# Optimization experiments

Hardware: AMD Instinct MI355X
Metric: run time of the kernel (lower is better)

## Reference

```python
import jax, jax.numpy as jnp
import numpy as np


def setup_inputs() -> dict:
    key = jax.random.key(0)
    ks = jax.random.split(key, 8)
    B = 32768
    return {
        "x": jax.random.normal(ks[0], (B, 784), dtype=jnp.float32),
        "conv_w": jax.random.normal(ks[1], (3, 3), dtype=jnp.float32),
        "fc1_w": jax.random.normal(ks[2], (512, 676), dtype=jnp.float32) * 0.04,
        "fc1_b": jax.random.normal(ks[3], (512,), dtype=jnp.float32),
        "fc2_w": jax.random.normal(ks[4], (512, 512), dtype=jnp.float32) * 0.04,
        "fc2_b": jax.random.normal(ks[5], (512,), dtype=jnp.float32),
        "out_w": jax.random.normal(ks[6], (10, 512), dtype=jnp.float32) * 0.04,
        "out_b": jax.random.normal(ks[7], (10,), dtype=jnp.float32),
    }


def reference(x, conv_w, fc1_w, fc1_b, fc2_w, fc2_b, out_w, out_b):
    B = x.shape[0]
    img = x.reshape(B, 1, 28, 28)  # NCHW, single channel
    # Valid 3x3 cross-correlation (same math as the nested tensordot loop).
    kern = conv_w.reshape(1, 1, 3, 3)  # OIHW
    conv = jax.lax.conv_general_dilated(
        img, kern, window_strides=(1, 1), padding="VALID",
        dimension_numbers=("NCHW", "OIHW", "NCHW"))  # [B,1,26,26]
    h = conv.reshape(B, 26 * 26)
    h = jax.nn.relu(h @ fc1_w.T + fc1_b)
    h = jax.nn.relu(h @ fc2_w.T + fc2_b)
    return h @ out_w.T + out_b  # [B,10] logits
```

## Files before the change

### kernel.cpp

```cpp
#include <hip/hip_runtime.h>

typedef unsigned short ushort_t;
typedef __attribute__((ext_vector_type(8))) short bf16x8;
typedef __attribute__((ext_vector_type(4))) float f32x4;
typedef __attribute__((ext_vector_type(16))) float f32x16;

__device__ __forceinline__ unsigned short f2bf(float f) {
    union { float f; unsigned u; } v; v.f = f;
    unsigned r = v.u + 0x7FFFu + ((v.u >> 16) & 1u);
    return (unsigned short)(r >> 16);
}

__device__ __forceinline__ unsigned cvt_pk_bf16(float a, float b) {
    unsigned r;
    asm("v_cvt_pk_bf16_f32 %0, %1, %2" : "=v"(r) : "v"(a), "v"(b));
    return r;
}

__global__ __launch_bounds__(256) void prep_w(const float* __restrict__ fc1_w,
                                              const float* __restrict__ cw,
                                              const float* __restrict__ fc2_w,
                                              const float* __restrict__ out_w,
                                              ushort_t* __restrict__ W1,
                                              ushort_t* __restrict__ W2,
                                              ushort_t* __restrict__ W3) {
    const int idx = blockIdx.x * 256 + threadIdx.x;
    if (idx < 425984) {
        const int ngrp = idx / 26624;
        const int kfrag = (idx % 26624) >> 9;
        const int li = idx & 511;
        const int lane = li >> 3, e = li & 7;
        const int n = ngrp * 32 + (lane & 31);
        const int p = kfrag * 16 + (lane >> 5) * 8 + e;
        float acc = 0.f;
        if (p < 784) {
            const int pr = p / 28, pc = p % 28;
            const float* frow = &fc1_w[n * 676];
#pragma unroll
            for (int dr = 0; dr < 3; ++dr) {
                const int r = pr - dr;
                const bool rok = (unsigned)r < 26u;
                const int rc = rok ? r : 0;
#pragma unroll
                for (int dc = 0; dc < 3; ++dc) {
                    const int c = pc - dc;
                    const bool cok = (unsigned)c < 26u;
                    const int cc = cok ? c : 0;
                    const float w = (rok && cok) ? cw[dr * 3 + dc] : 0.f;
                    acc += w * frow[rc * 26 + cc];
                }
            }
        }
        W1[idx] = f2bf(acc);
    }
    if (idx < 262144) {
        const int ngrp = idx / 16384;
        const int kfrag = (idx % 16384) >> 9;
        const int li = idx & 511;
        const int lane = li >> 3, e = li & 7;
        const int n = ngrp * 32 + (lane & 31);
        const int p = kfrag * 16 + (lane >> 5) * 8 + e;
        W2[idx] = f2bf(fc2_w[n * 512 + p]);
    }
    if (idx < 16 * 512)  W3[idx] = (idx < 10 * 512) ? f2bf(out_w[idx]) : (ushort_t)0;
}

__global__ __launch_bounds__(1024, 8) void mega10(const float* __restrict__ x,
                                                  const ushort_t* __restrict__ W1,
                                                  const ushort_t* __restrict__ W2,
                                                  const ushort_t* __restrict__ W3,
                                                  const float* __restrict__ b1,
                                                  const float* __restrict__ b2,
                                                  const float* __restrict__ ob,
                                                  float* __restrict__ out) {
    extern __shared__ ushort_t smem[];
    ushort_t* xs0 = smem;
    ushort_t* hs  = smem + 4096;

    const int tid = threadIdx.x;
    const int wave = tid >> 6, lane = tid & 63;
    const int r32 = lane & 31, khalf = lane >> 5;
    const int xrow = tid >> 4, xseg = tid & 15;
    const int m0 = blockIdx.x * 64;
    const size_t ng = wave;

    const float* xgp = &x[(size_t)(m0 + xrow) * 784 + xseg * 4];
    const int xldso = xrow * 64 + (((xseg >> 1) ^ (xrow & 7)) * 8) + (xseg & 1) * 4;

    f32x16 acc[2];
#pragma unroll
    for (int a = 0; a < 2; ++a)
#pragma unroll
        for (int e = 0; e < 16; ++e) acc[a][e] = 0.f;

    f32x4 xv;
    unsigned xlo, xhi;
    auto load_x = [&](int ks) {
        const int gc = ks * 64 + xseg * 4;
        if (gc < 784) {
            xv = __builtin_nontemporal_load((const f32x4*)(xgp + ks * 64));
        } else {
            xv = (f32x4){0.f, 0.f, 0.f, 0.f};
        }
    };
    auto cvt_x = [&]() {
        xlo = cvt_pk_bf16(xv.x, xv.y);
        xhi = cvt_pk_bf16(xv.z, xv.w);
    };
    auto write_x = [&](ushort_t* buf) {
        unsigned long long v = ((unsigned long long)xhi << 32) | xlo;
        *(unsigned long long*)&buf[xldso] = v;
    };

    auto write_h = [&](const float* __restrict__ bias) {
        const int n = wave * 32 + r32;
        const float bb = bias[n];
        const int nseg = n >> 3, nrem = n & 7;
#pragma unroll
        for (int i = 0; i < 2; ++i)
#pragma unroll
            for (int reg = 0; reg < 16; ++reg) {
                const int m = i * 32 + 4 * khalf + (reg & 3) + 8 * (reg >> 2);
                hs[m * 512 + ((nseg ^ (m & 7)) * 8) + nrem] = f2bf(fmaxf(acc[i][reg] + bb, 0.f));
            }
    };

    auto p1_ksub = [&](int kf, int ksub, const ushort_t* bufp) {
        const bf16x8 bw = *(const bf16x8*)&W1[(ng * 52 + kf) * 512 + lane * 8];
        const int q = 2 * ksub + khalf;
        bf16x8 af[2];
#pragma unroll
        for (int i = 0; i < 2; ++i) {
            const int m = i * 32 + r32;
            af[i] = *(const bf16x8*)&bufp[m * 64 + ((q ^ (m & 7)) * 8)];
        }
        __builtin_amdgcn_s_setprio(1);
        acc[0] = __builtin_amdgcn_mfma_f32_32x32x16_bf16(af[0], bw, acc[0], 0, 0, 0);
        acc[1] = __builtin_amdgcn_mfma_f32_32x32x16_bf16(af[1], bw, acc[1], 0, 0, 0);
        __builtin_amdgcn_s_setprio(0);
    };

    load_x(0);
    cvt_x();
    write_x(xs0);
    __syncthreads();

    for (int ks = 0; ks < 12; ++ks) {
        load_x(ks + 1);
        const ushort_t* bufp = (ks & 1) ? hs : xs0;
        p1_ksub(ks * 4 + 0, 0, bufp);
        p1_ksub(ks * 4 + 1, 1, bufp);
        p1_ksub(ks * 4 + 2, 2, bufp);
        cvt_x();
        p1_ksub(ks * 4 + 3, 3, bufp);
        write_x((ks & 1) ? xs0 : hs);
        __syncthreads();
    }
    {
        const ushort_t* bufp = xs0;
        const bf16x8 bw = *(const bf16x8*)&W1[(ng * 52 + 48) * 512 + lane * 8];
        const int q = khalf;
        bf16x8 af[2];
#pragma unroll
        for (int i = 0; i < 2; ++i) {
            const int m = i * 32 + r32;
            af[i] = *(const bf16x8*)&bufp[m * 64 + ((q ^ (m & 7)) * 8)];
        }
        __builtin_amdgcn_s_setprio(1);
        acc[0] = __builtin_amdgcn_mfma_f32_32x32x16_bf16(af[0], bw, acc[0], 0, 0, 0);
        acc[1] = __builtin_amdgcn_mfma_f32_32x32x16_bf16(af[1], bw, acc[1], 0, 0, 0);
        __builtin_amdgcn_s_setprio(0);
    }

    write_h(b1);
#pragma unroll
    for (int a = 0; a < 2; ++a)
#pragma unroll
        for (int e = 0; e < 16; ++e) acc[a][e] = 0.f;
    __syncthreads();

    for (int ks = 0; ks < 8; ++ks) {
#pragma unroll
        for (int ksub = 0; ksub < 4; ++ksub) {
            const int kf = ks * 4 + ksub;
            const bf16x8 bw = *(const bf16x8*)&W2[(ng * 32 + kf) * 512 + lane * 8];
            const int hq = kf * 2 + khalf;
            bf16x8 af[2];
#pragma unroll
            for (int i = 0; i < 2; ++i) {
                const int m = i * 32 + r32;
                af[i] = *(const bf16x8*)&hs[m * 512 + ((hq ^ (m & 7)) * 8)];
            }
            __builtin_amdgcn_s_setprio(1);
            acc[0] = __builtin_amdgcn_mfma_f32_32x32x16_bf16(af[0], bw, acc[0], 0, 0, 0);
            acc[1] = __builtin_amdgcn_mfma_f32_32x32x16_bf16(af[1], bw, acc[1], 0, 0, 0);
            __builtin_amdgcn_s_setprio(0);
        }
    }
    __syncthreads();

    write_h(b2);
    __syncthreads();

    if (wave < 4) {
        const int quad = lane >> 4, l16 = lane & 15;
        const int row = wave * 16 + l16;
        f32x4 hacc = {0.f, 0.f, 0.f, 0.f};
#pragma unroll
        for (int ks = 0; ks < 16; ++ks) {
            const int seg = 4 * ks + quad;
            const bf16x8 a = *(const bf16x8*)&hs[row * 512 + ((seg ^ (row & 7)) * 8)];
            const bf16x8 b = *(const bf16x8*)&W3[l16 * 512 + ks * 32 + quad * 8];
            hacc = __builtin_amdgcn_mfma_f32_16x16x32_bf16(a, b, hacc, 0, 0, 0);
        }
        if (l16 < 10) {
            const float bb = ob[l16];
#pragma unroll
            for (int r = 0; r < 4; ++r)
                out[(size_t)(m0 + wave * 16 + quad * 4 + r) * 10 + l16] = hacc[r] + bb;
        }
    }
}

extern "C" void kernel_launch(void* const* d_in, const int* in_sizes, int n_in,
                              void* d_out, int out_size, void* d_ws, size_t ws_size,
                              hipStream_t stream) {
    const float* x      = (const float*)d_in[0];
    const float* conv_w = (const float*)d_in[1];
    const float* fc1_w  = (const float*)d_in[2];
    const float* fc1_b  = (const float*)d_in[3];
    const float* fc2_w  = (const float*)d_in[4];
    const float* fc2_b  = (const float*)d_in[5];
    const float* out_w  = (const float*)d_in[6];
    const float* out_b  = (const float*)d_in[7];
    float* out = (float*)d_out;

    ushort_t* W1 = (ushort_t*)d_ws;
    ushort_t* W2 = W1 + 425984;
    ushort_t* W3 = W2 + 262144;

    prep_w<<<dim3(1664), 256, 0, stream>>>(fc1_w, conv_w, fc2_w, out_w, W1, W2, W3);

    mega10<<<dim3(512), 1024, 73728, stream>>>(x, W1, W2, W3, fc1_b, fc2_b, out_b, out);
}
```

Measured before the change: 213.0 us.

## Halve rows per block to 32 to double blocks and cut LDS

Each block now handles 32 batch rows instead of 64. That halves shared memory to 36 KB and doubles the grid to 1024 blocks, so more blocks can be resident per CU. Each wave now issues one MFMA per k-fragment instead of two, so every weight fragment loaded from global memory is reused across half as many rows, roughly doubling weight traffic. The loop body is also restructured to load four weight and four activation fragments up front before the MFMA chain.

```diff
diff --git a/kernel.cpp b/kernel.cpp
--- a/kernel.cpp
+++ b/kernel.cpp
@@ -2,6 +2,7 @@
 
 typedef unsigned short ushort_t;
 typedef __attribute__((ext_vector_type(8))) short bf16x8;
+typedef __attribute__((ext_vector_type(2))) float f32x2;
 typedef __attribute__((ext_vector_type(4))) float f32x4;
 typedef __attribute__((ext_vector_type(16))) float f32x16;
 
@@ -65,7 +66,7 @@
     if (idx < 16 * 512)  W3[idx] = (idx < 10 * 512) ? f2bf(out_w[idx]) : (ushort_t)0;
 }
 
-__global__ __launch_bounds__(1024, 8) void mega10(const float* __restrict__ x,
+__global__ __launch_bounds__(1024, 8) void mega11(const float* __restrict__ x,
                                                   const ushort_t* __restrict__ W1,
                                                   const ushort_t* __restrict__ W2,
                                                   const ushort_t* __restrict__ W3,
@@ -75,41 +76,33 @@
                                                   float* __restrict__ out) {
     extern __shared__ ushort_t smem[];
     ushort_t* xs0 = smem;
-    ushort_t* hs  = smem + 4096;
+    ushort_t* hs  = smem + 2048;
 
     const int tid = threadIdx.x;
     const int wave = tid >> 6, lane = tid & 63;
     const int r32 = lane & 31, khalf = lane >> 5;
-    const int xrow = tid >> 4, xseg = tid & 15;
-    const int m0 = blockIdx.x * 64;
+    const int xrow = tid >> 5, xc2 = (tid & 31) * 2;
+    const int m0 = blockIdx.x * 32;
     const size_t ng = wave;
 
-    const float* xgp = &x[(size_t)(m0 + xrow) * 784 + xseg * 4];
-    const int xldso = xrow * 64 + (((xseg >> 1) ^ (xrow & 7)) * 8) + (xseg & 1) * 4;
-
-    f32x16 acc[2];
-#pragma unroll
-    for (int a = 0; a < 2; ++a)
-#pragma unroll
-        for (int e = 0; e < 16; ++e) acc[a][e] = 0.f;
-
-    f32x4 xv;
-    unsigned xlo, xhi;
+    const float* xgp = &x[(size_t)(m0 + xrow) * 784 + xc2];
+    const int xldso = xrow * 64 + (((xc2 >> 3) ^ (xrow & 7)) * 8) + (xc2 & 7);
+
+    f32x16 acc;
+#pragma unroll
+    for (int e = 0; e < 16; ++e) acc[e] = 0.f;
+
+    f32x2 xv;
     auto load_x = [&](int ks) {
-        const int gc = ks * 64 + xseg * 4;
+        const int gc = ks * 64 + xc2;
         if (gc < 784) {
-            xv = __builtin_nontemporal_load((const f32x4*)(xgp + ks * 64));
+            xv = __builtin_nontemporal_load((const f32x2*)(xgp + ks * 64));
         } else {
-            xv = (f32x4){0.f, 0.f, 0.f, 0.f};
-        }
-    };
-    auto cvt_x = [&]() {
-        xlo = cvt_pk_bf16(xv.x, xv.y);
-        xhi = cvt_pk_bf16(xv.z, xv.w);
+            xv = (f32x2){0.f, 0.f};
+        }
     };
     auto write_x = [&](ushort_t* buf) {
-        unsigned long long v = ((unsigned long long)xhi << 32) | xlo;
-        *(unsigned long long*)&buf[xldso] = v;
+        *(unsigned*)&buf[xldso] = cvt_pk_bf16(xv.x, xv.y);
     };
 
     auto write_h = [&](const float* __restrict__ bias) {
@@ -117,92 +110,76 @@
         const float bb = bias[n];
         const int nseg = n >> 3, nrem = n & 7;
 #pragma unroll
-        for (int i = 0; i < 2; ++i)
-#pragma unroll
-            for (int reg = 0; reg < 16; ++reg) {
-                const int m = i * 32 + 4 * khalf + (reg & 3) + 8 * (reg >> 2);
-                hs[m * 512 + ((nseg ^ (m & 7)) * 8) + nrem] = f2bf(fmaxf(acc[i][reg] + bb, 0.f));
-            }
+        for (int reg = 0; reg < 16; ++reg) {
+            const int m = 4 * khalf + (reg & 3) + 8 * (reg >> 2);
+            hs[m * 512 + ((nseg ^ (m & 7)) * 8) + nrem] = f2bf(fmaxf(acc[reg] + bb, 0.f));
+        }
     };
 
-    auto p1_ksub = [&](int kf, int ksub, const ushort_t* bufp) {
-        const bf16x8 bw = *(const bf16x8*)&W1[(ng * 52 + kf) * 512 + lane * 8];
-        const int q = 2 * ksub + khalf;
-        bf16x8 af[2];
-#pragma unroll
-        for (int i = 0; i < 2; ++i) {
-            const int m = i * 32 + r32;
-            af[i] = *(const bf16x8*)&bufp[m * 64 + ((q ^ (m & 7)) * 8)];
-        }
-        __builtin_amdgcn_s_setprio(1);
-        acc[0] = __builtin_amdgcn_mfma_f32_32x32x16_bf16(af[0], bw, acc[0], 0, 0, 0);
-        acc[1] = __builtin_amdgcn_mfma_f32_32x32x16_bf16(af[1], bw, acc[1], 0, 0, 0);
-        __builtin_amdgcn_s_setprio(0);
-    };
-
     load_x(0);
-    cvt_x();
     write_x(xs0);
     __syncthreads();
 
     for (int ks = 0; ks < 12; ++ks) {
         load_x(ks + 1);
         const ushort_t* bufp = (ks & 1) ? hs : xs0;
-        p1_ksub(ks * 4 + 0, 0, bufp);
-        p1_ksub(ks * 4 + 1, 1, bufp);
-        p1_ksub(ks * 4 + 2, 2, bufp);
-        cvt_x();
-        p1_ksub(ks * 4 + 3, 3, bufp);
+        const ushort_t* wp = &W1[(ng * 52 + ks * 4) * 512 + lane * 8];
+        const int ro = r32 * 64, sw = r32 & 7;
+        const bf16x8 bw0 = *(const bf16x8*)(wp);
+        const bf16x8 bw1 = *(const bf16x8*)(wp + 512);
+        const bf16x8 bw2 = *(const bf16x8*)(wp + 1024);
+        const bf16x8 bw3 = *(const bf16x8*)(wp + 1536);
+        const bf16x8 a0 = *(const bf16x8*)&bufp[ro + (((0 + khalf) ^ sw) * 8)];
+        const bf16x8 a1 = *(const bf16x8*)&bufp[ro + (((2 + khalf) ^ sw) * 8)];
+        const bf16x8 a2 = *(const bf16x8*)&bufp[ro + (((4 + khalf) ^ sw) * 8)];
+        const bf16x8 a3 = *(const bf16x8*)&bufp[ro + (((6 + khalf) ^ sw) * 8)];
+        __builtin_amdgcn_s_setprio(1);
+        acc = __builtin_amdgcn_mfma_f32_32x32x16_bf16(a0, bw0, acc, 0, 0, 0);
+        acc = __builtin_amdgcn_mfma_f32_32x32x16_bf16(a1, bw1, acc, 0, 0, 0);
+        acc = __builtin_amdgcn_mfma_f32_32x32x16_bf16(a2, bw2, acc, 0, 0, 0);
+        acc = __builtin_amdgcn_mfma_f32_32x32x16_bf16(a3, bw3, acc, 0, 0, 0);
+        __builtin_amdgcn_s_setprio(0);
         write_x((ks & 1) ? xs0 : hs);
         __syncthreads();
     }
     {
         const ushort_t* bufp = xs0;
         const bf16x8 bw = *(const bf16x8*)&W1[(ng * 52 + 48) * 512 + lane * 8];
-        const int q = khalf;
-        bf16x8 af[2];
-#pragma unroll
-        for (int i = 0; i < 2; ++i) {
-            const int m = i * 32 + r32;
-            af[i] = *(const bf16x8*)&bufp[m * 64 + ((q ^ (m & 7)) * 8)];
-        }
+        const bf16x8 a0 = *(const bf16x8*)&bufp[r32 * 64 + ((khalf ^ (r32 & 7)) * 8)];
         __builtin_amdgcn_s_setprio(1);
-        acc[0] = __builtin_amdgcn_mfma_f32_32x32x16_bf16(af[0], bw, acc[0], 0, 0, 0);
-        acc[1] = __builtin_amdgcn_mfma_f32_32x32x16_bf16(af[1], bw, acc[1], 0, 0, 0);
+        acc = __builtin_amdgcn_mfma_f32_32x32x16_bf16(a0, bw, acc, 0, 0, 0);
         __builtin_amdgcn_s_setprio(0);
     }
 
     write_h(b1);
 #pragma unroll
-    for (int a = 0; a < 2; ++a)
-#pragma unroll
-        for (int e = 0; e < 16; ++e) acc[a][e] = 0.f;
+    for (int e = 0; e < 16; ++e) acc[e] = 0.f;
     __syncthreads();
 
     for (int ks = 0; ks < 8; ++ks) {
-#pragma unroll
-        for (int ksub = 0; ksub < 4; ++ksub) {
-            const int kf = ks * 4 + ksub;
-            const bf16x8 bw = *(const bf16x8*)&W2[(ng * 32 + kf) * 512 + lane * 8];
-            const int hq = kf * 2 + khalf;
-            bf16x8 af[2];
-#pragma unroll
-            for (int i = 0; i < 2; ++i) {
-                const int m = i * 32 + r32;
-                af[i] = *(const bf16x8*)&hs[m * 512 + ((hq ^ (m & 7)) * 8)];
-            }
-            __builtin_amdgcn_s_setprio(1);
-            acc[0] = __builtin_amdgcn_mfma_f32_32x32x16_bf16(af[0], bw, acc[0], 0, 0, 0);
-            acc[1] = __builtin_amdgcn_mfma_f32_32x32x16_bf16(af[1], bw, acc[1], 0, 0, 0);
-            __builtin_amdgcn_s_setprio(0);
-        }
+        const ushort_t* wp = &W2[(ng * 32 + ks * 4) * 512 + lane * 8];
+        const int ro = r32 * 512, sw = r32 & 7, hq0 = ks * 8 + khalf;
+        const bf16x8 bw0 = *(const bf16x8*)(wp);
+        const bf16x8 bw1 = *(const bf16x8*)(wp + 512);
+        const bf16x8 bw2 = *(const bf16x8*)(wp + 1024);
+        const bf16x8 bw3 = *(const bf16x8*)(wp + 1536);
+        const bf16x8 a0 = *(const bf16x8*)&hs[ro + (((hq0 + 0) ^ sw) * 8)];
+        const bf16x8 a1 = *(const bf16x8*)&hs[ro + (((hq0 + 2) ^ sw) * 8)];
+        const bf16x8 a2 = *(const bf16x8*)&hs[ro + (((hq0 + 4) ^ sw) * 8)];
+        const bf16x8 a3 = *(const bf16x8*)&hs[ro + (((hq0 + 6) ^ sw) * 8)];
+        __builtin_amdgcn_s_setprio(1);
+        acc = __builtin_amdgcn_mfma_f32_32x32x16_bf16(a0, bw0, acc, 0, 0, 0);
+        acc = __builtin_amdgcn_mfma_f32_32x32x16_bf16(a1, bw1, acc, 0, 0, 0);
+        acc = __builtin_amdgcn_mfma_f32_32x32x16_bf16(a2, bw2, acc, 0, 0, 0);
+        acc = __builtin_amdgcn_mfma_f32_32x32x16_bf16(a3, bw3, acc, 0, 0, 0);
+        __builtin_amdgcn_s_setprio(0);
     }
     __syncthreads();
 
     write_h(b2);
     __syncthreads();
 
-    if (wave < 4) {
+    if (wave < 2) {
         const int quad = lane >> 4, l16 = lane & 15;
         const int row = wave * 16 + l16;
         f32x4 hacc = {0.f, 0.f, 0.f, 0.f};
@@ -241,5 +218,5 @@
 
     prep_w<<<dim3(1664), 256, 0, stream>>>(fc1_w, conv_w, fc2_w, out_w, W1, W2, W3);
 
-    mega10<<<dim3(512), 1024, 73728, stream>>>(x, W1, W2, W3, fc1_b, fc2_b, out_b, out);
-}
+    mega11<<<dim3(1024), 1024, 36864, stream>>>(x, W1, W2, W3, fc1_b, fc2_b, out_b, out);
+}
```

After: 250.4 us. +17.6%, slower.

## Shrink block tile to 32 rows with 8 waves each owning two N-tiles

Applied to the files above, without the earlier changes.

Changes the fused MLP kernel from 64-row blocks with 16 waves (one 32-column N tile each) to 32-row blocks with 8 waves that each own two N tiles. Blocks drop to 512 threads and use half the shared memory, and the grid doubles to 1024 blocks. This is meant to improve occupancy and grid balance and to shorten barrier stalls. In exchange, every weight fragment from W1 and W2 is now reused across only 32 rows instead of 64, which doubles total weight traffic from L2.

```diff
diff --git a/kernel.cpp b/kernel.cpp
--- a/kernel.cpp
+++ b/kernel.cpp
@@ -65,36 +65,35 @@
     if (idx < 16 * 512)  W3[idx] = (idx < 10 * 512) ? f2bf(out_w[idx]) : (ushort_t)0;
 }
 
-__global__ __launch_bounds__(1024, 8) void mega10(const float* __restrict__ x,
-                                                  const ushort_t* __restrict__ W1,
-                                                  const ushort_t* __restrict__ W2,
-                                                  const ushort_t* __restrict__ W3,
-                                                  const float* __restrict__ b1,
-                                                  const float* __restrict__ b2,
-                                                  const float* __restrict__ ob,
-                                                  float* __restrict__ out) {
+__global__ __launch_bounds__(512, 6) void mega12(const float* __restrict__ x,
+                                                 const ushort_t* __restrict__ W1,
+                                                 const ushort_t* __restrict__ W2,
+                                                 const ushort_t* __restrict__ W3,
+                                                 const float* __restrict__ b1,
+                                                 const float* __restrict__ b2,
+                                                 const float* __restrict__ ob,
+                                                 float* __restrict__ out) {
     extern __shared__ ushort_t smem[];
     ushort_t* xs0 = smem;
-    ushort_t* hs  = smem + 4096;
+    ushort_t* hs  = smem + 2048;
 
     const int tid = threadIdx.x;
     const int wave = tid >> 6, lane = tid & 63;
     const int r32 = lane & 31, khalf = lane >> 5;
     const int xrow = tid >> 4, xseg = tid & 15;
-    const int m0 = blockIdx.x * 64;
-    const size_t ng = wave;
+    const int m0 = blockIdx.x * 32;
+    const size_t ng0 = wave * 2, ng1 = wave * 2 + 1;
 
     const float* xgp = &x[(size_t)(m0 + xrow) * 784 + xseg * 4];
     const int xldso = xrow * 64 + (((xseg >> 1) ^ (xrow & 7)) * 8) + (xseg & 1) * 4;
 
     f32x16 acc[2];
 #pragma unroll
-    for (int a = 0; a < 2; ++a)
-#pragma unroll
-        for (int e = 0; e < 16; ++e) acc[a][e] = 0.f;
+    for (int j = 0; j < 2; ++j)
+#pragma unroll
+        for (int e = 0; e < 16; ++e) acc[j][e] = 0.f;
 
     f32x4 xv;
-    unsigned xlo, xhi;
     auto load_x = [&](int ks) {
         const int gc = ks * 64 + xseg * 4;
         if (gc < 784) {
@@ -103,45 +102,39 @@
             xv = (f32x4){0.f, 0.f, 0.f, 0.f};
         }
     };
-    auto cvt_x = [&]() {
-        xlo = cvt_pk_bf16(xv.x, xv.y);
-        xhi = cvt_pk_bf16(xv.z, xv.w);
-    };
     auto write_x = [&](ushort_t* buf) {
-        unsigned long long v = ((unsigned long long)xhi << 32) | xlo;
-        *(unsigned long long*)&buf[xldso] = v;
+        const unsigned lo = cvt_pk_bf16(xv.x, xv.y);
+        const unsigned hi = cvt_pk_bf16(xv.z, xv.w);
+        unsigned* p = (unsigned*)&buf[xldso];
+        p[0] = lo; p[1] = hi;
     };
 
     auto write_h = [&](const float* __restrict__ bias) {
-        const int n = wave * 32 + r32;
-        const float bb = bias[n];
-        const int nseg = n >> 3, nrem = n & 7;
-#pragma unroll
-        for (int i = 0; i < 2; ++i)
+#pragma unroll
+        for (int j = 0; j < 2; ++j) {
+            const int n = (wave * 2 + j) * 32 + r32;
+            const float bb = bias[n];
+            const int nseg = n >> 3, nrem = n & 7;
 #pragma unroll
             for (int reg = 0; reg < 16; ++reg) {
-                const int m = i * 32 + 4 * khalf + (reg & 3) + 8 * (reg >> 2);
-                hs[m * 512 + ((nseg ^ (m & 7)) * 8) + nrem] = f2bf(fmaxf(acc[i][reg] + bb, 0.f));
+                const int m = 4 * khalf + (reg & 3) + 8 * (reg >> 2);
+                hs[m * 512 + ((nseg ^ (m & 7)) * 8) + nrem] = f2bf(fmaxf(acc[j][reg] + bb, 0.f));
             }
+        }
     };
 
     auto p1_ksub = [&](int kf, int ksub, const ushort_t* bufp) {
-        const bf16x8 bw = *(const bf16x8*)&W1[(ng * 52 + kf) * 512 + lane * 8];
+        const bf16x8 bw0 = *(const bf16x8*)&W1[(ng0 * 52 + kf) * 512 + lane * 8];
+        const bf16x8 bw1 = *(const bf16x8*)&W1[(ng1 * 52 + kf) * 512 + lane * 8];
         const int q = 2 * ksub + khalf;
-        bf16x8 af[2];
-#pragma unroll
-        for (int i = 0; i < 2; ++i) {
-            const int m = i * 32 + r32;
-            af[i] = *(const bf16x8*)&bufp[m * 64 + ((q ^ (m & 7)) * 8)];
-        }
+        const bf16x8 af = *(const bf16x8*)&bufp[r32 * 64 + ((q ^ (r32 & 7)) * 8)];
         __builtin_amdgcn_s_setprio(1);
-        acc[0] = __builtin_amdgcn_mfma_f32_32x32x16_bf16(af[0], bw, acc[0], 0, 0, 0);
-        acc[1] = __builtin_amdgcn_mfma_f32_32x32x16_bf16(af[1], bw, acc[1], 0, 0, 0);
+        acc[0] = __builtin_amdgcn_mfma_f32_32x32x16_bf16(af, bw0, acc[0], 0, 0, 0);
+        acc[1] = __builtin_amdgcn_mfma_f32_32x32x16_bf16(af, bw1, acc[1], 0, 0, 0);
         __builtin_amdgcn_s_setprio(0);
     };
 
     load_x(0);
-    cvt_x();
     write_x(xs0);
     __syncthreads();
 
@@ -151,49 +144,30 @@
         p1_ksub(ks * 4 + 0, 0, bufp);
         p1_ksub(ks * 4 + 1, 1, bufp);
         p1_ksub(ks * 4 + 2, 2, bufp);
-        cvt_x();
         p1_ksub(ks * 4 + 3, 3, bufp);
         write_x((ks & 1) ? xs0 : hs);
         __syncthreads();
     }
-    {
-        const ushort_t* bufp = xs0;
-        const bf16x8 bw = *(const bf16x8*)&W1[(ng * 52 + 48) * 512 + lane * 8];
-        const int q = khalf;
-        bf16x8 af[2];
-#pragma unroll
-        for (int i = 0; i < 2; ++i) {
-            const int m = i * 32 + r32;
-            af[i] = *(const bf16x8*)&bufp[m * 64 + ((q ^ (m & 7)) * 8)];
-        }
-        __builtin_amdgcn_s_setprio(1);
-        acc[0] = __builtin_amdgcn_mfma_f32_32x32x16_bf16(af[0], bw, acc[0], 0, 0, 0);
-        acc[1] = __builtin_amdgcn_mfma_f32_32x32x16_bf16(af[1], bw, acc[1], 0, 0, 0);
-        __builtin_amdgcn_s_setprio(0);
-    }
+    p1_ksub(48, 0, xs0);
 
     write_h(b1);
 #pragma unroll
-    for (int a = 0; a < 2; ++a)
-#pragma unroll
-        for (int e = 0; e < 16; ++e) acc[a][e] = 0.f;
+    for (int j = 0; j < 2; ++j)
+#pragma unroll
+        for (int e = 0; e < 16; ++e) acc[j][e] = 0.f;
     __syncthreads();
 
     for (int ks = 0; ks < 8; ++ks) {
 #pragma unroll
         for (int ksub = 0; ksub < 4; ++ksub) {
             const int kf = ks * 4 + ksub;
-            const bf16x8 bw = *(const bf16x8*)&W2[(ng * 32 + kf) * 512 + lane * 8];
+            const bf16x8 bw0 = *(const bf16x8*)&W2[(ng0 * 32 + kf) * 512 + lane * 8];
+            const bf16x8 bw1 = *(const bf16x8*)&W2[(ng1 * 32 + kf) * 512 + lane * 8];
             const int hq = kf * 2 + khalf;
-            bf16x8 af[2];
-#pragma unroll
-            for (int i = 0; i < 2; ++i) {
-                const int m = i * 32 + r32;
-                af[i] = *(const bf16x8*)&hs[m * 512 + ((hq ^ (m & 7)) * 8)];
-            }
+            const bf16x8 af = *(const bf16x8*)&hs[r32 * 512 + ((hq ^ (r32 & 7)) * 8)];
             __builtin_amdgcn_s_setprio(1);
-            acc[0] = __builtin_amdgcn_mfma_f32_32x32x16_bf16(af[0], bw, acc[0], 0, 0, 0);
-            acc[1] = __builtin_amdgcn_mfma_f32_32x32x16_bf16(af[1], bw, acc[1], 0, 0, 0);
+            acc[0] = __builtin_amdgcn_mfma_f32_32x32x16_bf16(af, bw0, acc[0], 0, 0, 0);
+            acc[1] = __builtin_amdgcn_mfma_f32_32x32x16_bf16(af, bw1, acc[1], 0, 0, 0);
             __builtin_amdgcn_s_setprio(0);
         }
     }
@@ -202,7 +176,7 @@
     write_h(b2);
     __syncthreads();
 
-    if (wave < 4) {
+    if (wave < 2) {
         const int quad = lane >> 4, l16 = lane & 15;
         const int row = wave * 16 + l16;
         f32x4 hacc = {0.f, 0.f, 0.f, 0.f};
@@ -241,5 +215,5 @@
 
     prep_w<<<dim3(1664), 256, 0, stream>>>(fc1_w, conv_w, fc2_w, out_w, W1, W2, W3);
 
-    mega10<<<dim3(512), 1024, 73728, stream>>>(x, W1, W2, W3, fc1_b, fc2_b, out_b, out);
-}
+    mega12<<<dim3(1024), 512, 36864, stream>>>(x, W1, W2, W3, fc1_b, fc2_b, out_b, out);
+}
```

Measured after the change: 220.8 us. 3.7% more time.
